# Performance work log

Hardware: AMD Instinct MI355X
Metric: run time of the kernel (lower is better)

## Reference

```python
import jax, jax.numpy as jnp
import numpy as np

VOCAB = 30
EMBED = 256          # forced equal to 2*KVS by weight tying
KVS = 128            # key_value_size
B = 128
T_ENC = 1024
MAX_LEN = 250


def setup_inputs() -> dict:
    key0 = jax.random.key(0)
    ks = jax.random.split(key0, 10)
    return {
        "key": jax.random.normal(ks[0], (B, T_ENC, KVS), jnp.float32),
        "value": jax.random.normal(ks[1], (B, T_ENC, KVS), jnp.float32),
        "encoder_len": jax.random.randint(ks[2], (B,), 1, T_ENC),
        "y": jax.random.randint(ks[3], (B, MAX_LEN), 0, VOCAB),
        # learned params
        "emb": jax.random.normal(ks[4], (VOCAB, EMBED), jnp.float32) * 0.1,  # tied: embedding AND character_prob weight
        "W_ih": jax.random.normal(ks[5], (4 * KVS, EMBED + KVS), jnp.float32) * 0.05,
        "W_hh": jax.random.normal(ks[6], (4 * KVS, KVS), jnp.float32) * 0.05,
        "b_ih": jax.random.normal(ks[7], (4 * KVS,), jnp.float32) * 0.05,
        "b_hh": jax.random.normal(ks[8], (4 * KVS,), jnp.float32) * 0.05,
        "b_cp": jax.random.normal(ks[9], (VOCAB,), jnp.float32) * 0.05,
    }


def reference(key, value, encoder_len, y, emb, W_ih, W_hh, b_ih, b_hh, b_cp):
    # padding_idx=0: lookups of row 0 carry no gradient (value unchanged)
    emb_lookup = emb.at[0].set(jax.lax.stop_gradient(emb[0]))
    # teacher forcing: step 0 uses zeros, step i uses embedding of y[:, i-1]
    char_embeds = emb_lookup[y]                               # [B, L, E]
    shifted = jnp.concatenate(
        [jnp.zeros((B, 1, EMBED), char_embeds.dtype), char_embeds[:, :-1, :]], axis=1
    )                                                          # [B, L, E]
    xs = jnp.swapaxes(shifted, 0, 1)                           # [L, B, E]

    h0 = jnp.zeros((B, KVS), key.dtype)
    c0 = jnp.zeros((B, KVS), key.dtype)
    ctx0 = value[:, 0, :]                                      # [B, KVS]

    def step(carry, char_embed):
        h, c, ctx = carry
        x = jnp.concatenate([char_embed, ctx], axis=1)         # [B, E+KVS]
        gates = x @ W_ih.T + b_ih + h @ W_hh.T + b_hh          # [B, 4*KVS]
        i_g, f_g, g_g, o_g = jnp.split(gates, 4, axis=1)       # PyTorch LSTMCell gate order
        c_new = jax.nn.sigmoid(f_g) * c + jax.nn.sigmoid(i_g) * jnp.tanh(g_g)
        h_new = jax.nn.sigmoid(o_g) * jnp.tanh(c_new)
        query = h_new
        energy = jnp.einsum('btk,bk->bt', key, query)          # [B, T]
        attn = jax.nn.softmax(energy, axis=-1)
        ctx_new = jnp.einsum('bt,btk->bk', attn, value)        # [B, KVS]
        out_ctx = jnp.concatenate([query, ctx_new], axis=1)    # [B, 2*KVS]
        pred = out_ctx @ emb.T + b_cp                          # tied projection, [B, V]
        return (h_new, c_new, ctx_new), (pred, attn[0])

    _, (preds, attn0) = jax.lax.scan(step, (h0, c0, ctx0), xs)
    predictions = jnp.swapaxes(preds, 0, 1)                    # [B, L, V]
    attentions = attn0                                         # [L, T] (sample 0 per step)
    return predictions, attentions
```

## Files before the change

kernel.cpp:

```cpp
#include <hip/hip_runtime.h>

#define VOCAB   30
#define EMBED   256
#define KVS     128
#define BATCH   128
#define T_ENC   1024
#define MAX_LEN 250
#define NTH     1024
#define HALF_T  512

typedef unsigned int uint32;
typedef unsigned short ushort16;

__device__ __forceinline__ float dot4(float4 a, float4 b) {
  return a.x * b.x + a.y * b.y + a.z * b.z + a.w * b.w;
}
__device__ __forceinline__ float bf_lo(uint32 u) { return __uint_as_float(u << 16); }
__device__ __forceinline__ float bf_hi(uint32 u) { return __uint_as_float(u & 0xffff0000u); }
__device__ __forceinline__ ushort16 f2bf(float f) {
  uint32 u = __float_as_uint(f);
  return (ushort16)((u + 0x7FFFu + ((u >> 16) & 1u)) >> 16);
}
__device__ __forceinline__ uint32 pack2(float a, float b) {
  return (uint32)f2bf(a) | ((uint32)f2bf(b) << 16);
}
__device__ __forceinline__ void ws_store(float* p, float v) {
  __hip_atomic_store(p, v, __ATOMIC_RELAXED, __HIP_MEMORY_SCOPE_AGENT);
}
__device__ __forceinline__ float ws_load(const float* p) {
  return __hip_atomic_load(p, __ATOMIC_RELAXED, __HIP_MEMORY_SCOPE_AGENT);
}

__global__ __launch_bounds__(NTH, 4) void decoder_kernel(
    const float* __restrict__ key,
    const float* __restrict__ value,
    const int*   __restrict__ y,
    const float* __restrict__ emb,
    const float* __restrict__ W_ih,
    const float* __restrict__ W_hh,
    const float* __restrict__ b_ih,
    const float* __restrict__ b_hh,
    const float* __restrict__ b_cp,
    float* __restrict__ out,
    float* __restrict__ msgsA,
    float* __restrict__ msgsB,
    int*   __restrict__ flags)
{
  __shared__ uint32 s_V[HALF_T * 64];
  __shared__ ushort16 s_G16[VOCAB * 256];
  __shared__ __align__(16) float s_rec[256];
  __shared__ float s_gates[256];
  __shared__ float s_c[64];
  __shared__ float s_attn[HALF_T];
  __shared__ float s_part[16][KVS];
  __shared__ float s_redm[16];
  __shared__ float s_reds[16];
  __shared__ float s_stats[2];
  __shared__ float s_biasloc[256];
  __shared__ float s_bcp[VOCAB];
  __shared__ int   s_y[MAX_LEN];

  const int bid  = blockIdx.x;
  const int half = (bid >> 3) & 1;
  const int b    = (bid & 7) | ((bid >> 4) << 3);
  const int tid  = threadIdx.x;
  const int lane = tid & 63;
  const int wid  = tid >> 6;
  const int rloc = tid >> 2;
  const int q    = tid & 3;

  const float* keyb = key   + (size_t)b * T_ENC * KVS + (size_t)half * HALF_T * KVS;
  const float* valb = value + (size_t)b * T_ENC * KVS + (size_t)half * HALF_T * KVS;

  float* s_scr = (float*)s_V;
  for (int i = tid; i < VOCAB * EMBED; i += NTH) s_scr[i] = emb[i];
  for (int i = tid; i < MAX_LEN; i += NTH)       s_y[i] = y[b * MAX_LEN + i];
  if (tid < VOCAB) s_bcp[tid] = b_cp[tid];
  if (tid < 256) {
    const int g2 = tid >> 6, j2 = tid & 63;
    const int gr2 = g2 * 128 + half * 64 + j2;
    s_biasloc[tid] = b_ih[gr2] + b_hh[gr2];
  }
  if (tid < KVS) {
    s_rec[tid] = value[(size_t)b * T_ENC * KVS + tid];
    s_rec[128 + tid] = 0.f;
  }
  if (tid < 64) s_c[tid] = 0.f;
  __syncthreads();

  const int gate = rloc >> 6, jj = rloc & 63;
  const int grow = gate * 128 + half * 64 + jj;
  const float4* Wih4 = (const float4*)W_ih;
  const float4* Whh4 = (const float4*)W_hh;

  {
    float4 we[16];
    #pragma unroll
    for (int k = 0; k < 16; ++k) we[k] = Wih4[(size_t)grow * 96 + 4 * k + q];
    const float4* se4 = (const float4*)s_scr;
    for (int v = 0; v < VOCAB; ++v) {
      float a = 0.f;
      #pragma unroll
      for (int k = 0; k < 16; ++k) a += dot4(we[k], se4[v * 64 + 4 * k + q]);
      a += __shfl_xor(a, 1);
      a += __shfl_xor(a, 2);
      if (q == 0) s_G16[v * 256 + rloc] = f2bf(a + s_biasloc[rloc]);
    }
  }
  __syncthreads();

  float4 w4[16];
  #pragma unroll
  for (int k = 0; k < 8; ++k)
    w4[k] = Wih4[(size_t)grow * 96 + 64 + 4 * k + q];
  #pragma unroll
  for (int k = 8; k < 16; ++k)
    w4[k] = Whh4[(size_t)grow * 32 + 4 * (k - 8) + q];

  uint4 ku[8];
  {
    const float4* kg = (const float4*)(keyb + (size_t)(tid >> 1) * KVS + (tid & 1) * 64);
    #pragma unroll 2
    for (int i = 0; i < 8; ++i) {
      const float4 a0 = kg[2 * i], a1 = kg[2 * i + 1];
      ku[i].x = pack2(a0.x, a0.y); ku[i].y = pack2(a0.z, a0.w);
      ku[i].z = pack2(a1.x, a1.y); ku[i].w = pack2(a1.z, a1.w);
    }
  }

  for (int idx = tid; idx < HALF_T * 64; idx += NTH) {
    const int row = idx >> 6, cp = idx & 63;
    const float2 v2 = *(const float2*)(valb + (size_t)row * KVS + 2 * cp);
    s_V[idx] = pack2(v2.x, v2.y);
  }
  __syncthreads();

  const size_t PRED_SZ = (size_t)BATCH * MAX_LEN * VOCAB;
  const float4* sr4 = (const float4*)s_rec;

  for (int t = 0; t < MAX_LEN; ++t) {
    const int par = t & 1;
    float*       msgA_out = msgsA + (size_t)(((b * 2 + par) * 2) + half) * 64;
    const float* msgA_in  = msgsA + (size_t)(((b * 2 + par) * 2) + (half ^ 1)) * 64;
    float*       msgB_out = msgsB + (size_t)(((b * 2 + par) * 2) + half) * 130;
    const float* msgB_in  = msgsB + (size_t)(((b * 2 + par) * 2) + (half ^ 1)) * 130;
    int* flagA_out = flags + (((b * 2 + par) * 2 + 0) * 2) + half;
    int* flagA_in  = flags + (((b * 2 + par) * 2 + 0) * 2) + (half ^ 1);
    int* flagB_out = flags + (((b * 2 + par) * 2 + 1) * 2) + half;
    int* flagB_in  = flags + (((b * 2 + par) * 2 + 1) * 2) + (half ^ 1);

    {
      float a = 0.f;
      #pragma unroll
      for (int k = 0; k < 16; ++k) a += dot4(w4[k], sr4[4 * k + q]);
      a += __shfl_xor(a, 1);
      a += __shfl_xor(a, 2);
      if (q == 0) {
        const float gb = (t == 0)
            ? s_biasloc[rloc]
            : __uint_as_float(((uint32)s_G16[s_y[t - 1] * 256 + rloc]) << 16);
        s_gates[rloc] = a + gb;
      }
    }
    __syncthreads();

    if (tid < 64) {
      float ig = s_gates[tid], fg = s_gates[64 + tid];
      float gg = s_gates[128 + tid], og = s_gates[192 + tid];
      float si = 1.f / (1.f + __expf(-ig));
      float sf = 1.f / (1.f + __expf(-fg));
      float so = 1.f / (1.f + __expf(-og));
      float cn = sf * s_c[tid] + si * tanhf(gg);
      s_c[tid] = cn;
      float hn = so * tanhf(cn);
      s_rec[128 + half * 64 + tid] = hn;
      ws_store(msgA_out + tid, hn);
    }
    __syncthreads();
    if (tid == 0) {
      __hip_atomic_store(flagA_out, t + 1, __ATOMIC_RELEASE, __HIP_MEMORY_SCOPE_AGENT);
      while (__hip_atomic_load(flagA_in, __ATOMIC_ACQUIRE, __HIP_MEMORY_SCOPE_AGENT) < t + 1) {}
    }
    __syncthreads();
    if (tid < 64) s_rec[128 + (half ^ 1) * 64 + tid] = ws_load(msgA_in + tid);
    __syncthreads();

    {
      const int r = tid >> 1, kh = tid & 1;
      const float4* h4 = (const float4*)(s_rec + 128) + kh * 16;
      float a = 0.f;
      #pragma unroll 2
      for (int i = 0; i < 8; ++i) {
        const uint4 kw = ku[i];
        const float4 hA = h4[2 * i], hB = h4[2 * i + 1];
        a += bf_lo(kw.x) * hA.x + bf_hi(kw.x) * hA.y
           + bf_lo(kw.y) * hA.z + bf_hi(kw.y) * hA.w
           + bf_lo(kw.z) * hB.x + bf_hi(kw.z) * hB.y
           + bf_lo(kw.w) * hB.z + bf_hi(kw.w) * hB.w;
      }
      a += __shfl_xor(a, 1);
      if (kh == 0) s_attn[r] = a;
    }
    __syncthreads();

    float p_loc, m_loc, l_loc;
    {
      const float e = (tid < HALF_T) ? s_attn[tid] : -1e30f;
      float mm = e;
      #pragma unroll
      for (int o = 32; o; o >>= 1) mm = fmaxf(mm, __shfl_xor(mm, o));
      if (lane == 0) s_redm[wid] = mm;
      __syncthreads();
      m_loc = s_redm[0];
      #pragma unroll
      for (int w = 1; w < 16; ++w) m_loc = fmaxf(m_loc, s_redm[w]);
      float p = (tid < HALF_T) ? __expf(e - m_loc) : 0.f;
      p_loc = p;
      if (tid < HALF_T) s_attn[tid] = p;
      float ss = p;
      #pragma unroll
      for (int o = 32; o; o >>= 1) ss += __shfl_xor(ss, o);
      if (lane == 0) s_reds[wid] = ss;
      __syncthreads();
      l_loc = 0.f;
      #pragma unroll
      for (int w = 0; w < 16; ++w) l_loc += s_reds[w];
    }

    {
      const int cp = tid & 63, ch = wid;
      float ax = 0.f, ay = 0.f;
      #pragma unroll 8
      for (int r2 = 0; r2 < 32; ++r2) {
        const int row = ch + (r2 << 4);
        const float w = s_attn[row];
        const uint32 pv = s_V[(row << 6) + cp];
        ax += w * bf_lo(pv); ay += w * bf_hi(pv);
      }
      s_part[ch][2 * cp] = ax; s_part[ch][2 * cp + 1] = ay;
    }
    __syncthreads();
    float ctxp = 0.f;
    if (tid < KVS) {
      #pragma unroll
      for (int p2 = 0; p2 < 16; ++p2) ctxp += s_part[p2][tid];
    }

    if (tid < KVS)      ws_store(msgB_out + 2 + tid, ctxp);
    if (tid == KVS)     ws_store(msgB_out + 0, m_loc);
    if (tid == KVS + 1) ws_store(msgB_out + 1, l_loc);
    __syncthreads();
    if (tid == 0) {
      __hip_atomic_store(flagB_out, t + 1, __ATOMIC_RELEASE, __HIP_MEMORY_SCOPE_AGENT);
      while (__hip_atomic_load(flagB_in, __ATOMIC_ACQUIRE, __HIP_MEMORY_SCOPE_AGENT) < t + 1) {}
      s_stats[0] = ws_load(msgB_in + 0);
      s_stats[1] = ws_load(msgB_in + 1);
    }
    __syncthreads();
    const float m_rem = s_stats[0], l_rem = s_stats[1];
    const float mA = half ? m_rem : m_loc, mB = half ? m_loc : m_rem;
    const float lA = half ? l_rem : l_loc, lB = half ? l_loc : l_rem;
    const float M  = fmaxf(mA, mB);
    const float wA = __expf(mA - M), wB = __expf(mB - M);
    const float S  = wA * lA + wB * lB;
    const float invS = 1.f / S;
    const float w_own = half ? wB : wA;
    if (tid < KVS) {
      const float cr = ws_load(msgB_in + 2 + tid);
      const float cA = half ? cr : ctxp, cB = half ? ctxp : cr;
      s_rec[tid] = (wA * cA + wB * cB) * invS;
    }
    if (b == 0 && tid < HALF_T) {
      out[PRED_SZ + (size_t)t * T_ENC + half * HALF_T + tid] = p_loc * w_own * invS;
    }
    __syncthreads();

    if (half == 0 && tid < 480) {
      const int v = tid >> 4, sl = tid & 15;
      const float4* eg = (const float4*)(emb + v * EMBED + sl * 16);
      const float* oc = (sl < 8) ? (s_rec + 128 + sl * 16) : (s_rec + (sl - 8) * 16);
      float acc = dot4(eg[0], *(const float4*)(oc))
                + dot4(eg[1], *(const float4*)(oc + 4))
                + dot4(eg[2], *(const float4*)(oc + 8))
                + dot4(eg[3], *(const float4*)(oc + 12));
      #pragma unroll
      for (int o = 8; o; o >>= 1) acc += __shfl_xor(acc, o);
      if (sl == 0) out[((size_t)b * MAX_LEN + t) * VOCAB + v] = acc + s_bcp[v];
    }
  }
}

extern "C" void kernel_launch(void* const* d_in, const int* in_sizes, int n_in,
                              void* d_out, int out_size, void* d_ws, size_t ws_size,
                              hipStream_t stream) {
  const float* key   = (const float*)d_in[0];
  const float* value = (const float*)d_in[1];
  const int*   y     = (const int*)d_in[3];
  const float* emb   = (const float*)d_in[4];
  const float* W_ih  = (const float*)d_in[5];
  const float* W_hh  = (const float*)d_in[6];
  const float* b_ih  = (const float*)d_in[7];
  const float* b_hh  = (const float*)d_in[8];
  const float* b_cp  = (const float*)d_in[9];
  float* out = (float*)d_out;

  int*   flags = (int*)d_ws;
  float* msgsA = (float*)((char*)d_ws + 8192);
  float* msgsB = (float*)((char*)d_ws + 8192 + 131072);

  hipMemsetAsync(d_ws, 0, 8192, stream);
  decoder_kernel<<<2 * BATCH, NTH, 0, stream>>>(key, value, y, emb, W_ih, W_hh,
                                                b_ih, b_hh, b_cp, out,
                                                msgsA, msgsB, flags);
}
```

Before: 4.784 ms.

## Compute full LSTM gates redundantly per half to drop mid-step cross-block exchange

Each of the two blocks per batch row now computes all 512 gate rows and the full 128-wide hidden state itself, using bf16-packed W_ih/W_hh weights held in registers. This removes the first inter-block flag handshake and message exchange in every timestep. The embedding-times-W_ih lookup table moves to a separate prologue kernel in global memory, so the per-block precompute and the shared-memory G table go away. Flag synchronisation is relaxed from acquire/release to relaxed atomics. The cost is doubled gate work, lower weight precision, and a per-step global read of the G table, and the relaxed flags weaken memory ordering guarantees.

```diff
diff --git a/kernel.cpp b/kernel.cpp
--- a/kernel.cpp
+++ b/kernel.cpp
@@ -10,16 +10,16 @@
 #define HALF_T  512
 
 typedef unsigned int uint32;
-typedef unsigned short ushort16;
+typedef unsigned short u16;
 
 __device__ __forceinline__ float dot4(float4 a, float4 b) {
   return a.x * b.x + a.y * b.y + a.z * b.z + a.w * b.w;
 }
 __device__ __forceinline__ float bf_lo(uint32 u) { return __uint_as_float(u << 16); }
 __device__ __forceinline__ float bf_hi(uint32 u) { return __uint_as_float(u & 0xffff0000u); }
-__device__ __forceinline__ ushort16 f2bf(float f) {
+__device__ __forceinline__ u16 f2bf(float f) {
   uint32 u = __float_as_uint(f);
-  return (ushort16)((u + 0x7FFFu + ((u >> 16) & 1u)) >> 16);
+  return (u16)((u + 0x7FFFu + ((u >> 16) & 1u)) >> 16);
 }
 __device__ __forceinline__ uint32 pack2(float a, float b) {
   return (uint32)f2bf(a) | ((uint32)f2bf(b) << 16);
@@ -29,6 +29,27 @@
 }
 __device__ __forceinline__ float ws_load(const float* p) {
   return __hip_atomic_load(p, __ATOMIC_RELAXED, __HIP_MEMORY_SCOPE_AGENT);
+}
+__device__ __forceinline__ void flag_store(int* p, int v) {
+  __hip_atomic_store(p, v, __ATOMIC_RELAXED, __HIP_MEMORY_SCOPE_AGENT);
+}
+__device__ __forceinline__ int flag_load(const int* p) {
+  return __hip_atomic_load(p, __ATOMIC_RELAXED, __HIP_MEMORY_SCOPE_AGENT);
+}
+
+__global__ void build_G(const float* __restrict__ emb, const float* __restrict__ W_ih,
+                        const float* __restrict__ b_ih, const float* __restrict__ b_hh,
+                        float* __restrict__ G) {
+  const int v = blockIdx.x;
+  const int r = threadIdx.x;
+  float acc = b_ih[r] + b_hh[r];
+  if (v < VOCAB) {
+    const float4* w = (const float4*)(W_ih + (size_t)r * 384);
+    const float4* e = (const float4*)(emb + (size_t)v * EMBED);
+    #pragma unroll 8
+    for (int k = 0; k < 64; ++k) acc += dot4(w[k], e[k]);
+  }
+  G[v * 512 + r] = acc;
 }
 
 __global__ __launch_bounds__(NTH, 4) void decoder_kernel(
@@ -38,25 +59,21 @@
     const float* __restrict__ emb,
     const float* __restrict__ W_ih,
     const float* __restrict__ W_hh,
-    const float* __restrict__ b_ih,
-    const float* __restrict__ b_hh,
     const float* __restrict__ b_cp,
+    const float* __restrict__ G_tab,
     float* __restrict__ out,
-    float* __restrict__ msgsA,
-    float* __restrict__ msgsB,
+    float* __restrict__ msgs,
     int*   __restrict__ flags)
 {
   __shared__ uint32 s_V[HALF_T * 64];
-  __shared__ ushort16 s_G16[VOCAB * 256];
   __shared__ __align__(16) float s_rec[256];
-  __shared__ float s_gates[256];
-  __shared__ float s_c[64];
-  __shared__ float s_attn[HALF_T];
+  __shared__ float s_gates[512];
+  __shared__ float s_attn[512];
+  __shared__ float s_c[128];
   __shared__ float s_part[16][KVS];
   __shared__ float s_redm[16];
   __shared__ float s_reds[16];
   __shared__ float s_stats[2];
-  __shared__ float s_biasloc[256];
   __shared__ float s_bcp[VOCAB];
   __shared__ int   s_y[MAX_LEN];
 
@@ -66,60 +83,35 @@
   const int tid  = threadIdx.x;
   const int lane = tid & 63;
   const int wid  = tid >> 6;
-  const int rloc = tid >> 2;
-  const int q    = tid & 3;
+  const int rr   = tid >> 1;
+  const int cc   = tid & 1;
 
   const float* keyb = key   + (size_t)b * T_ENC * KVS + (size_t)half * HALF_T * KVS;
   const float* valb = value + (size_t)b * T_ENC * KVS + (size_t)half * HALF_T * KVS;
 
-  float* s_scr = (float*)s_V;
-  for (int i = tid; i < VOCAB * EMBED; i += NTH) s_scr[i] = emb[i];
-  for (int i = tid; i < MAX_LEN; i += NTH)       s_y[i] = y[b * MAX_LEN + i];
+  for (int i = tid; i < MAX_LEN; i += NTH) s_y[i] = y[b * MAX_LEN + i];
   if (tid < VOCAB) s_bcp[tid] = b_cp[tid];
-  if (tid < 256) {
-    const int g2 = tid >> 6, j2 = tid & 63;
-    const int gr2 = g2 * 128 + half * 64 + j2;
-    s_biasloc[tid] = b_ih[gr2] + b_hh[gr2];
-  }
   if (tid < KVS) {
     s_rec[tid] = value[(size_t)b * T_ENC * KVS + tid];
     s_rec[128 + tid] = 0.f;
   }
-  if (tid < 64) s_c[tid] = 0.f;
-  __syncthreads();
-
-  const int gate = rloc >> 6, jj = rloc & 63;
-  const int grow = gate * 128 + half * 64 + jj;
-  const float4* Wih4 = (const float4*)W_ih;
-  const float4* Whh4 = (const float4*)W_hh;
-
+  if (tid < 128) s_c[tid] = 0.f;
+
+  uint4 gw[16];
   {
-    float4 we[16];
-    #pragma unroll
-    for (int k = 0; k < 16; ++k) we[k] = Wih4[(size_t)grow * 96 + 4 * k + q];
-    const float4* se4 = (const float4*)s_scr;
-    for (int v = 0; v < VOCAB; ++v) {
-      float a = 0.f;
-      #pragma unroll
-      for (int k = 0; k < 16; ++k) a += dot4(we[k], se4[v * 64 + 4 * k + q]);
-      a += __shfl_xor(a, 1);
-      a += __shfl_xor(a, 2);
-      if (q == 0) s_G16[v * 256 + rloc] = f2bf(a + s_biasloc[rloc]);
-    }
-  }
-  __syncthreads();
-
-  float4 w4[16];
-  #pragma unroll
-  for (int k = 0; k < 8; ++k)
-    w4[k] = Wih4[(size_t)grow * 96 + 64 + 4 * k + q];
-  #pragma unroll
-  for (int k = 8; k < 16; ++k)
-    w4[k] = Whh4[(size_t)grow * 32 + 4 * (k - 8) + q];
+    const float4* p = (cc == 0) ? (const float4*)(W_ih + (size_t)rr * 384 + 256)
+                                : (const float4*)(W_hh + (size_t)rr * 128);
+    #pragma unroll 4
+    for (int k = 0; k < 16; ++k) {
+      const float4 a0 = p[2 * k], a1 = p[2 * k + 1];
+      gw[k].x = pack2(a0.x, a0.y); gw[k].y = pack2(a0.z, a0.w);
+      gw[k].z = pack2(a1.x, a1.y); gw[k].w = pack2(a1.z, a1.w);
+    }
+  }
 
   uint4 ku[8];
   {
-    const float4* kg = (const float4*)(keyb + (size_t)(tid >> 1) * KVS + (tid & 1) * 64);
+    const float4* kg = (const float4*)(keyb + (size_t)rr * KVS + cc * 64);
     #pragma unroll 2
     for (int i = 0; i < 8; ++i) {
       const float4 a0 = kg[2 * i], a1 = kg[2 * i + 1];
@@ -140,54 +132,43 @@
 
   for (int t = 0; t < MAX_LEN; ++t) {
     const int par = t & 1;
-    float*       msgA_out = msgsA + (size_t)(((b * 2 + par) * 2) + half) * 64;
-    const float* msgA_in  = msgsA + (size_t)(((b * 2 + par) * 2) + (half ^ 1)) * 64;
-    float*       msgB_out = msgsB + (size_t)(((b * 2 + par) * 2) + half) * 130;
-    const float* msgB_in  = msgsB + (size_t)(((b * 2 + par) * 2) + (half ^ 1)) * 130;
-    int* flagA_out = flags + (((b * 2 + par) * 2 + 0) * 2) + half;
-    int* flagA_in  = flags + (((b * 2 + par) * 2 + 0) * 2) + (half ^ 1);
-    int* flagB_out = flags + (((b * 2 + par) * 2 + 1) * 2) + half;
-    int* flagB_in  = flags + (((b * 2 + par) * 2 + 1) * 2) + (half ^ 1);
-
-    {
+    float*       msg_out = msgs + (size_t)(((b * 2 + par) * 2) + half) * 130;
+    const float* msg_in  = msgs + (size_t)(((b * 2 + par) * 2) + (half ^ 1)) * 130;
+    int* flag_out = flags + ((b * 2 + par) * 2) + half;
+    int* flag_in  = flags + ((b * 2 + par) * 2) + (half ^ 1);
+
+    {
+      const int yprev = (t == 0) ? VOCAB : s_y[t - 1];
+      const float gb = G_tab[yprev * 512 + rr];
       float a = 0.f;
       #pragma unroll
-      for (int k = 0; k < 16; ++k) a += dot4(w4[k], sr4[4 * k + q]);
+      for (int k = 0; k < 16; ++k) {
+        const uint4 w = gw[k];
+        const float4 xA = sr4[cc * 32 + 2 * k], xB = sr4[cc * 32 + 2 * k + 1];
+        a += bf_lo(w.x) * xA.x + bf_hi(w.x) * xA.y
+           + bf_lo(w.y) * xA.z + bf_hi(w.y) * xA.w
+           + bf_lo(w.z) * xB.x + bf_hi(w.z) * xB.y
+           + bf_lo(w.w) * xB.z + bf_hi(w.w) * xB.w;
+      }
       a += __shfl_xor(a, 1);
-      a += __shfl_xor(a, 2);
-      if (q == 0) {
-        const float gb = (t == 0)
-            ? s_biasloc[rloc]
-            : __uint_as_float(((uint32)s_G16[s_y[t - 1] * 256 + rloc]) << 16);
-        s_gates[rloc] = a + gb;
-      }
-    }
-    __syncthreads();
-
-    if (tid < 64) {
-      float ig = s_gates[tid], fg = s_gates[64 + tid];
-      float gg = s_gates[128 + tid], og = s_gates[192 + tid];
-      float si = 1.f / (1.f + __expf(-ig));
-      float sf = 1.f / (1.f + __expf(-fg));
-      float so = 1.f / (1.f + __expf(-og));
-      float cn = sf * s_c[tid] + si * tanhf(gg);
+      if (cc == 0) s_gates[rr] = a + gb;
+    }
+    __syncthreads();
+
+    if (tid < 128) {
+      const float ig = s_gates[tid],       fg = s_gates[128 + tid];
+      const float gg = s_gates[256 + tid], og = s_gates[384 + tid];
+      const float si = 1.f / (1.f + __expf(-ig));
+      const float sf = 1.f / (1.f + __expf(-fg));
+      const float so = 1.f / (1.f + __expf(-og));
+      const float cn = sf * s_c[tid] + si * tanhf(gg);
       s_c[tid] = cn;
-      float hn = so * tanhf(cn);
-      s_rec[128 + half * 64 + tid] = hn;
-      ws_store(msgA_out + tid, hn);
-    }
-    __syncthreads();
-    if (tid == 0) {
-      __hip_atomic_store(flagA_out, t + 1, __ATOMIC_RELEASE, __HIP_MEMORY_SCOPE_AGENT);
-      while (__hip_atomic_load(flagA_in, __ATOMIC_ACQUIRE, __HIP_MEMORY_SCOPE_AGENT) < t + 1) {}
-    }
-    __syncthreads();
-    if (tid < 64) s_rec[128 + (half ^ 1) * 64 + tid] = ws_load(msgA_in + tid);
-    __syncthreads();
-
-    {
-      const int r = tid >> 1, kh = tid & 1;
-      const float4* h4 = (const float4*)(s_rec + 128) + kh * 16;
+      s_rec[128 + tid] = so * tanhf(cn);
+    }
+    __syncthreads();
+
+    {
+      const float4* h4 = (const float4*)(s_rec + 128) + cc * 16;
       float a = 0.f;
       #pragma unroll 2
       for (int i = 0; i < 8; ++i) {
@@ -199,7 +180,7 @@
            + bf_lo(kw.w) * hB.z + bf_hi(kw.w) * hB.w;
       }
       a += __shfl_xor(a, 1);
-      if (kh == 0) s_attn[r] = a;
+      if (cc == 0) s_attn[rr] = a;
     }
     __syncthreads();
 
@@ -214,7 +195,7 @@
       m_loc = s_redm[0];
       #pragma unroll
       for (int w = 1; w < 16; ++w) m_loc = fmaxf(m_loc, s_redm[w]);
-      float p = (tid < HALF_T) ? __expf(e - m_loc) : 0.f;
+      const float p = (tid < HALF_T) ? __expf(e - m_loc) : 0.f;
       p_loc = p;
       if (tid < HALF_T) s_attn[tid] = p;
       float ss = p;
@@ -246,15 +227,15 @@
       for (int p2 = 0; p2 < 16; ++p2) ctxp += s_part[p2][tid];
     }
 
-    if (tid < KVS)      ws_store(msgB_out + 2 + tid, ctxp);
-    if (tid == KVS)     ws_store(msgB_out + 0, m_loc);
-    if (tid == KVS + 1) ws_store(msgB_out + 1, l_loc);
+    if (tid < KVS)      ws_store(msg_out + 2 + tid, ctxp);
+    if (tid == KVS)     ws_store(msg_out + 0, m_loc);
+    if (tid == KVS + 1) ws_store(msg_out + 1, l_loc);
     __syncthreads();
     if (tid == 0) {
-      __hip_atomic_store(flagB_out, t + 1, __ATOMIC_RELEASE, __HIP_MEMORY_SCOPE_AGENT);
-      while (__hip_atomic_load(flagB_in, __ATOMIC_ACQUIRE, __HIP_MEMORY_SCOPE_AGENT) < t + 1) {}
-      s_stats[0] = ws_load(msgB_in + 0);
-      s_stats[1] = ws_load(msgB_in + 1);
+      flag_store(flag_out, t + 1);
+      while (flag_load(flag_in) < t + 1) {}
+      s_stats[0] = ws_load(msg_in + 0);
+      s_stats[1] = ws_load(msg_in + 1);
     }
     __syncthreads();
     const float m_rem = s_stats[0], l_rem = s_stats[1];
@@ -266,7 +247,7 @@
     const float invS = 1.f / S;
     const float w_own = half ? wB : wA;
     if (tid < KVS) {
-      const float cr = ws_load(msgB_in + 2 + tid);
+      const float cr = ws_load(msg_in + 2 + tid);
       const float cA = half ? cr : ctxp, cB = half ? ctxp : cr;
       s_rec[tid] = (wA * cA + wB * cB) * invS;
     }
@@ -305,11 +286,11 @@
   float* out = (float*)d_out;
 
   int*   flags = (int*)d_ws;
-  float* msgsA = (float*)((char*)d_ws + 8192);
-  float* msgsB = (float*)((char*)d_ws + 8192 + 131072);
+  float* msgs  = (float*)((char*)d_ws + 8192);
+  float* G_tab = (float*)((char*)d_ws + (1u << 19));
 
   hipMemsetAsync(d_ws, 0, 8192, stream);
+  build_G<<<VOCAB + 1, 512, 0, stream>>>(emb, W_ih, b_ih, b_hh, G_tab);
   decoder_kernel<<<2 * BATCH, NTH, 0, stream>>>(key, value, y, emb, W_ih, W_hh,
-                                                b_ih, b_hh, b_cp, out,
-                                                msgsA, msgsB, flags);
-}
+                                                b_cp, G_tab, out, msgs, flags);
+}
```

Measured after the change: 4.222 ms. 11.7% less time.
